# Kernel tuning notes

Measured on AMD Instinct MI355X. Metric: run time of the kernel, lower is better.

The kernel has to match this reference:

```python
import jax, jax.numpy as jnp
import numpy as np

B, Q, DIN, DOUT = 1, 1024, 4096, 4096
H, G, HD = 32, 8, 128          # heads, kv groups, head_dim; group_size = H // G
PREV = 3072                     # cached KV length
MAXPOS = 4096                   # rope table length (>= PREV + Q)
START = PREV


def _rope_tables(max_pos, head_dim):
    half = head_dim // 2
    inv_freq = 1.0 / (10000.0 ** (jnp.arange(half, dtype=jnp.float32) / half))
    ang = jnp.arange(max_pos, dtype=jnp.float32)[:, None] * inv_freq[None, :]
    ang = jnp.concatenate([ang, ang], axis=-1)  # [max_pos, head_dim]
    return jnp.cos(ang), jnp.sin(ang)


def apply_rope(x, cos, sin, start_pos):
    # x: [b, h, s, d]; rotate-half RoPE with absolute positions start_pos..start_pos+s
    s, d = x.shape[2], x.shape[3]
    c = cos[start_pos:start_pos + s]  # [s, d] (start_pos is a Python int)
    sn = sin[start_pos:start_pos + s]
    x1, x2 = x[..., : d // 2], x[..., d // 2:]
    rotated = jnp.concatenate([-x2, x1], axis=-1)
    return x * c + rotated * sn


def setup_inputs() -> dict:
    key = jax.random.key(0)
    ks = jax.random.split(key, 7)
    x = jax.random.normal(ks[0], (B, Q, DIN), dtype=jnp.float32)
    cos, sin = _rope_tables(MAXPOS, HD)
    # causal mask: query at abs position START+i may attend kv position j <= START+i
    qpos = START + jnp.arange(Q)
    kpos = jnp.arange(START + Q)
    mask = (kpos[None, :] > qpos[:, None])[None, None]  # [1,1,Q,KV], True = masked
    prev_k = jax.random.normal(ks[1], (B, G, PREV, HD), dtype=jnp.float32)
    prev_v = jax.random.normal(ks[2], (B, G, PREV, HD), dtype=jnp.float32)
    sc = 0.02
    Wq = jax.random.normal(ks[3], (DIN, DOUT), dtype=jnp.float32) * sc
    Wk = jax.random.normal(ks[4], (DIN, G * HD), dtype=jnp.float32) * sc
    Wv = jax.random.normal(ks[5], (DIN, G * HD), dtype=jnp.float32) * sc
    Wo = jax.random.normal(ks[6], (DOUT, DOUT), dtype=jnp.float32) * sc
    return dict(x=x, mask=mask, cos=cos, sin=sin, start_pos=START,
                prev_k=prev_k, prev_v=prev_v, Wq=Wq, Wk=Wk, Wv=Wv, Wo=Wo)


def reference(x, mask, cos, sin, start_pos, prev_k, prev_v, Wq, Wk, Wv, Wo):
    b, s, _ = x.shape
    gs = H // G  # group_size
    q = (x @ Wq).reshape(b, s, H, HD).transpose(0, 2, 1, 3)   # [b,H,s,hd]
    k = (x @ Wk).reshape(b, s, G, HD).transpose(0, 2, 1, 3)   # [b,G,s,hd]
    v = (x @ Wv).reshape(b, s, G, HD).transpose(0, 2, 1, 3)
    q = apply_rope(q, cos, sin, start_pos)
    k = apply_rope(k, cos, sin, start_pos)
    keys = jnp.concatenate([prev_k, k], axis=2)    # [b,G,KV,hd]
    values = jnp.concatenate([prev_v, v], axis=2)
    # grouped attention (equivalent to repeat_interleave of K/V over group_size)
    qg = q.reshape(b, G, gs, s, HD)
    scores = jnp.einsum('bgnqd,bgkd->bgnqk', qg, keys)        # [b,G,gs,s,KV]
    scores = jnp.where(mask[:, :, None], -jnp.inf, scores)
    attn = jax.nn.softmax(scores / np.sqrt(HD).astype(np.float32), axis=-1)
    ctx = jnp.einsum('bgnqk,bgkd->bgnqd', attn, values)       # [b,G,gs,s,hd]
    ctx = ctx.reshape(b, H, s, HD).transpose(0, 2, 1, 3).reshape(b, s, DOUT)
    out = ctx @ Wo
    return (out, keys, values)
```

## Files before the change

kernel.cpp:

```cpp
#include <hip/hip_runtime.h>
#include <hip/hip_bf16.h>

typedef unsigned short u16;
typedef unsigned int u32;
typedef __attribute__((ext_vector_type(4))) float f32x4;
typedef __attribute__((ext_vector_type(16))) float f32x16;
typedef __attribute__((ext_vector_type(8))) __bf16 bf16x8;
typedef __attribute__((ext_vector_type(4))) u16 u16x4;
typedef __attribute__((ext_vector_type(8))) u16 u16x8;
typedef __attribute__((ext_vector_type(4))) u32 u32x4;

#define START_POS 3072
#define NKV 4096
#define HD_ 128
#define SEQ 1024
#define DIN_ 4096
#define DQKV 6144

__device__ __forceinline__ void gll16(const void* g, void* l) {
  __builtin_amdgcn_global_load_lds((const __attribute__((address_space(1))) u32*)g,
                                   (__attribute__((address_space(3))) u32*)l, 16, 0, 0);
}
__device__ __forceinline__ u16 f2bf(float f) {
  u32 u = __builtin_bit_cast(u32, f);
  return (u16)((u + 0x7fffu + ((u >> 16) & 1u)) >> 16);
}
__device__ __forceinline__ u32 pack2bf(float a, float b) {
  __hip_bfloat162 t = __float22bfloat162_rn(float2{a, b});
  u32 u; __builtin_memcpy(&u, &t, 4);
  return u;
}
__device__ __forceinline__ f32x4 mfma16(bf16x8 a, bf16x8 b, f32x4 c) {
  return __builtin_amdgcn_mfma_f32_16x16x32_bf16(a, b, c, 0, 0, 0);
}
__device__ __forceinline__ f32x16 mfma32(bf16x8 a, bf16x8 b, f32x16 c) {
  return __builtin_amdgcn_mfma_f32_32x32x16_bf16(a, b, c, 0, 0, 0);
}

__global__ __launch_bounds__(256) void wtrans(const float* __restrict__ W,
    u16* __restrict__ Wt, int N, int ntn, int row_off)
{
  __shared__ float T[64][68];
  int bid = blockIdx.x;
  int nt = bid % ntn, kt = bid / ntn;
  int t = threadIdx.x;
  int kl = t >> 4, nl4 = (t & 15) << 2;
#pragma unroll
  for (int r = 0; r < 4; r++) {
    int row = r * 16 + kl;
    f32x4 v = *(const f32x4*)(W + (size_t)(kt * 64 + row) * N + nt * 64 + nl4);
    T[row][nl4] = v[0]; T[row][nl4 + 1] = v[1]; T[row][nl4 + 2] = v[2]; T[row][nl4 + 3] = v[3];
  }
  __syncthreads();
  int nl = t >> 2, k0 = (t & 3) << 4;
  u16x8 lo, hi;
#pragma unroll
  for (int j = 0; j < 8; j++) lo[j] = f2bf(T[k0 + j][nl]);
#pragma unroll
  for (int j = 0; j < 8; j++) hi[j] = f2bf(T[k0 + 8 + j][nl]);
  u16* dst = Wt + (size_t)(row_off + nt * 64 + nl) * 4096 + kt * 64 + k0;
  *(u16x8*)dst = lo;
  *(u16x8*)(dst + 8) = hi;
}

__global__ __launch_bounds__(256) void cvt_bf16(const float* __restrict__ src,
    u16* __restrict__ dst, int n4)
{
  int i = blockIdx.x * 256 + threadIdx.x;
  if (i >= n4) return;
  f32x4 v = *(const f32x4*)(src + (size_t)i * 4);
  u16x4 o;
#pragma unroll
  for (int j = 0; j < 4; j++) o[j] = f2bf(v[j]);
  *(u16x4*)(dst + (size_t)i * 4) = o;
}

__global__ __launch_bounds__(256) void gemm_bt(
    const u16* __restrict__ A, const u16* __restrict__ Bt,
    float* __restrict__ C, int N, int K, int nbx)
{
  __shared__ u16 As[2 * 128 * 64];
  __shared__ u16 Bs[2 * 64 * 64];
  int nwg = (int)gridDim.x;
  int orig = blockIdx.x;
  int q8 = nwg >> 3, r8 = nwg & 7;
  int xcd = orig & 7, jj = orig >> 3;
  int wgid = (xcd < r8 ? xcd * (q8 + 1) : r8 * (q8 + 1) + (xcd - r8) * q8) + jj;
  int by = wgid / nbx, bx = wgid % nbx;
  int tid = threadIdx.x, lane = tid & 63, wid = tid >> 6;
  int wr = wid >> 1, wc = wid & 1;
  int c = lane & 15, hh = lane >> 4;
  int srow = lane >> 3;
  int schunk = ((lane & 7) ^ srow) << 3;
  const u16* aS0 = A + (size_t)(by * 128 + wid * 32 + srow) * K + schunk;
  const u16* bS0 = Bt + (size_t)(bx * 64 + wid * 16 + srow) * K + schunk;

#define GSTAGE(buf, kk) do { \
  _Pragma("unroll") \
  for (int r = 0; r < 4; r++) \
    gll16(aS0 + (size_t)r * 8 * K + (kk), As + (buf) * 8192 + (wid * 32 + r * 8) * 64); \
  _Pragma("unroll") \
  for (int r = 0; r < 2; r++) \
    gll16(bS0 + (size_t)r * 8 * K + (kk), Bs + (buf) * 4096 + (wid * 16 + r * 8) * 64); \
} while (0)

  f32x4 acc[4][2] = {};
  int nk = K >> 6;
  int cur = 0;
  int rsl = c & 7;
  GSTAGE(0, 0);
  __syncthreads();
  for (int kt = 0; kt < nk; kt++) {
    if (kt + 1 < nk) GSTAGE(cur ^ 1, (kt + 1) * 64);
    const u16* Ab = As + cur * 8192;
    const u16* Bb = Bs + cur * 4096;
#pragma unroll
    for (int kk = 0; kk < 2; kk++) {
      int slot = ((kk * 4 + hh) ^ rsl) * 8;
      bf16x8 af[4], bf[2];
#pragma unroll
      for (int i = 0; i < 4; i++)
        af[i] = *(const bf16x8*)(Ab + (wr * 64 + i * 16 + c) * 64 + slot);
#pragma unroll
      for (int i = 0; i < 2; i++)
        bf[i] = *(const bf16x8*)(Bb + (wc * 32 + i * 16 + c) * 64 + slot);
      __builtin_amdgcn_s_setprio(1);
#pragma unroll
      for (int mi = 0; mi < 4; mi++)
#pragma unroll
        for (int ni = 0; ni < 2; ni++)
          acc[mi][ni] = mfma16(af[mi], bf[ni], acc[mi][ni]);
      __builtin_amdgcn_s_setprio(0);
    }
    __syncthreads();
    cur ^= 1;
  }
#undef GSTAGE
  int row0 = by * 128 + wr * 64 + hh * 4;
  int col0 = bx * 64 + wc * 32 + c;
#pragma unroll
  for (int mi = 0; mi < 4; mi++)
#pragma unroll
    for (int ni = 0; ni < 2; ni++)
#pragma unroll
      for (int i = 0; i < 4; i++)
        C[(size_t)(row0 + mi * 16 + i) * N + col0 + ni * 16] = acc[mi][ni][i];
}

__global__ __launch_bounds__(256) void rope_q(const float* __restrict__ qkv,
    const float* __restrict__ cosb, const float* __restrict__ sinb, u16* __restrict__ qb)
{
  const float C2 = 0.12751744f;
  int tid = blockIdx.x * 256 + threadIdx.x;
  int dq = tid & 15, h = (tid >> 4) & 31, s = tid >> 9;
  int d = dq << 2;
  const float* base = qkv + (size_t)s * DQKV + h * HD_ + d;
  f32x4 a = *(const f32x4*)base;
  f32x4 b2 = *(const f32x4*)(base + 64);
  f32x4 cc = *(const f32x4*)(cosb + (size_t)(START_POS + s) * HD_ + d);
  f32x4 sn = *(const f32x4*)(sinb + (size_t)(START_POS + s) * HD_ + d);
  u16x4 o1, o2;
#pragma unroll
  for (int i = 0; i < 4; i++) {
    o1[i] = f2bf((a[i] * cc[i] - b2[i] * sn[i]) * C2);
    o2[i] = f2bf((b2[i] * cc[i] + a[i] * sn[i]) * C2);
  }
  u16* dst = qb + ((size_t)h * SEQ + s) * HD_ + d;
  *(u16x4*)dst = o1;
  *(u16x4*)(dst + 64) = o2;
}

__global__ __launch_bounds__(256) void rope_k(const float* __restrict__ qkv,
    const float* __restrict__ cosb, const float* __restrict__ sinb,
    float* __restrict__ keys, u16* __restrict__ kbb)
{
  int tid = blockIdx.x * 256 + threadIdx.x;
  int dq = tid & 15, g = (tid >> 4) & 7, s = tid >> 7;
  int d = dq << 2;
  const float* base = qkv + (size_t)s * DQKV + DIN_ + g * HD_ + d;
  f32x4 a = *(const f32x4*)base;
  f32x4 b2 = *(const f32x4*)(base + 64);
  f32x4 cc = *(const f32x4*)(cosb + (size_t)(START_POS + s) * HD_ + d);
  f32x4 sn = *(const f32x4*)(sinb + (size_t)(START_POS + s) * HD_ + d);
  f32x4 o1, o2;
  u16x4 p1, p2;
#pragma unroll
  for (int i = 0; i < 4; i++) {
    o1[i] = a[i] * cc[i] - b2[i] * sn[i];
    o2[i] = b2[i] * cc[i] + a[i] * sn[i];
    p1[i] = f2bf(o1[i]);
    p2[i] = f2bf(o2[i]);
  }
  size_t off = ((size_t)g * NKV + START_POS + s) * HD_ + d;
  *(f32x4*)(keys + off) = o1;
  *(f32x4*)(keys + off + 64) = o2;
  *(u16x4*)(kbb + off) = p1;
  *(u16x4*)(kbb + off + 64) = p2;
}

__global__ __launch_bounds__(256) void copy_vnew(const float* __restrict__ qkv,
    float* __restrict__ values)
{
  int tid = blockIdx.x * 256 + threadIdx.x;
  int dq = tid & 31, g = (tid >> 5) & 7, s = tid >> 8;
  int d = dq << 2;
  f32x4 v = *(const f32x4*)(qkv + (size_t)s * DQKV + DIN_ + 1024 + g * HD_ + d);
  *(f32x4*)(values + ((size_t)g * NKV + START_POS + s) * HD_ + d) = v;
}

__global__ __launch_bounds__(256) void prev_copy(const float* __restrict__ pk,
    const float* __restrict__ pv, float* __restrict__ keys, float* __restrict__ values,
    u16* __restrict__ kbb)
{
  int idx = blockIdx.x * 256 + threadIdx.x;
  int d4 = idx & 31;
  int rest = idx >> 5;
  int p = rest % 3072, g = rest / 3072;
  f32x4 kq = *(const f32x4*)(pk + (size_t)idx * 4);
  f32x4 vq = *(const f32x4*)(pv + (size_t)idx * 4);
  size_t off = ((size_t)g * NKV + p) * HD_ + d4 * 4;
  *(f32x4*)(keys + off) = kq;
  *(f32x4*)(values + off) = vq;
  u16x4 kb4;
#pragma unroll
  for (int i = 0; i < 4; i++) kb4[i] = f2bf(kq[i]);
  *(u16x4*)(kbb + off) = kb4;
}

__global__ __launch_bounds__(256) void vtrans(const float* __restrict__ pv,
    const float* __restrict__ qkv, u16* __restrict__ vT)
{
  __shared__ float T[64][68];
  int bid = blockIdx.x;
  int dt = bid & 1, pt = (bid >> 1) & 63, g = bid >> 7;
  int t = threadIdx.x;
  int pl = t >> 4, dl4 = (t & 15) << 2;
#pragma unroll
  for (int r = 0; r < 4; r++) {
    int row = r * 16 + pl;
    int pos = pt * 64 + row;
    f32x4 v;
    if (pos < START_POS)
      v = *(const f32x4*)(pv + ((size_t)g * START_POS + pos) * HD_ + dt * 64 + dl4);
    else
      v = *(const f32x4*)(qkv + (size_t)(pos - START_POS) * DQKV + 5120 + g * HD_ + dt * 64 + dl4);
    T[row][dl4] = v[0]; T[row][dl4 + 1] = v[1]; T[row][dl4 + 2] = v[2]; T[row][dl4 + 3] = v[3];
  }
  __syncthreads();
  int dl = t >> 2, p0 = (t & 3) << 4;
  u16x8 lo, hi;
#pragma unroll
  for (int j = 0; j < 8; j++) lo[j] = f2bf(T[p0 + j][dl]);
#pragma unroll
  for (int j = 0; j < 8; j++) hi[j] = f2bf(T[p0 + 8 + j][dl]);
  u16* dst = vT + ((size_t)g * HD_ + dt * 64 + dl) * NKV + pt * 64 + p0;
  *(u16x8*)dst = lo;
  *(u16x8*)(dst + 8) = hi;
}

__global__ __launch_bounds__(128, 2) void attn_fwd(
    const u16* __restrict__ qb, const u16* __restrict__ kb,
    const u16* __restrict__ vT, float* __restrict__ Opart, float* __restrict__ Ml)
{
  __shared__ u16 Ks[2 * 32 * 128];
  __shared__ u16 Vs[2 * 128 * 32];
  int bid = blockIdx.x;
  int g = bid & 7, j = bid >> 3;
  int sp = j >> 6, jj = j & 63;
  int h = g * 4 + (jj >> 4), qt = jj & 15;
  int tid = threadIdx.x, lane = tid & 63, w = tid >> 6;
  int c32 = lane & 31, h8 = lane >> 5;
  int qw0 = qt * 64 + w * 32;
  bf16x8 Qf[8];
#pragma unroll
  for (int dc = 0; dc < 8; dc++)
    Qf[dc] = *(const bf16x8*)(qb + ((size_t)(h * 1024 + qw0 + c32)) * 128 + dc * 16 + h8 * 8);
  f32x16 O0 = {}, O1 = {}, O2 = {}, O3 = {};
  float Mx = -1e30f, Ls = 0.f;
  int t0 = sp ? (49 + qt) : 0;
  int t1 = sp ? (98 + 2 * qt) : (49 + qt);

#define STAGE_KV(tt, bo) do { \
  _Pragma("unroll") \
  for (int r = 0; r < 4; r++) { \
    int s = w * 256 + r * 64 + lane; \
    int krow = s >> 4, sl = s & 15; \
    gll16(kb + ((size_t)(g * 4096 + (tt) * 32 + krow)) * 128 + (sl ^ (krow & 7)) * 8, \
          Ks + (bo) + (w * 256 + r * 64) * 8); \
    int d = s >> 2, sl2 = s & 3; \
    gll16(vT + ((size_t)(g * 128 + d)) * 4096 + (tt) * 32 + (sl2 ^ ((d >> 1) & 3)) * 8, \
          Vs + (bo) + (w * 256 + r * 64) * 8); \
  } \
} while (0)

  int cur = 0;
  STAGE_KV(t0, 0);
  __syncthreads();
  int vxr = (c32 >> 1) & 3;
  for (int t = t0; t < t1; t++) {
    if (t + 1 < t1) STAGE_KV(t + 1, (cur ^ 1) * 4096);
    const u16* Kb = Ks + cur * 4096;
    const u16* Vb = Vs + cur * 4096;
    f32x16 S0 = {}, Sb = {};
    __builtin_amdgcn_s_setprio(1);
#pragma unroll
    for (int dc = 0; dc < 8; dc += 2) {
      int sxA = (2 * dc + h8) ^ (c32 & 7);
      int sxB = (2 * dc + 2 + h8) ^ (c32 & 7);
      bf16x8 kA = *(const bf16x8*)(Kb + (size_t)c32 * 128 + sxA * 8);
      bf16x8 kB = *(const bf16x8*)(Kb + (size_t)c32 * 128 + sxB * 8);
      S0 = mfma32(kA, Qf[dc], S0);
      Sb = mfma32(kB, Qf[dc + 1], Sb);
    }
    __builtin_amdgcn_s_setprio(0);
#pragma unroll
    for (int r = 0; r < 16; r++) S0[r] += Sb[r];
    if (t * 32 + 31 > START_POS + qw0) {
      int qa = START_POS + qw0 + c32;
#pragma unroll
      for (int r = 0; r < 16; r++) {
        int kvo = t * 32 + (r & 3) + 8 * (r >> 2) + 4 * h8;
        if (kvo > qa) S0[r] = -1e30f;
      }
    }
    float tm[16];
#pragma unroll
    for (int r = 0; r < 16; r++) tm[r] = S0[r];
#pragma unroll
    for (int sft = 8; sft >= 1; sft >>= 1)
#pragma unroll
      for (int r = 0; r < sft; r++) tm[r] = fmaxf(tm[r], tm[r + sft]);
    float full = fmaxf(tm[0], __shfl_xor(tm[0], 32));
    if (!__all(full <= Mx + 8.0f)) {
      float Mn = fmaxf(Mx, full);
      float al = exp2f(Mx - Mn);
      Mx = Mn;
      Ls *= al;
#pragma unroll
      for (int r = 0; r < 16; r++) { O0[r] *= al; O1[r] *= al; O2[r] *= al; O3[r] *= al; }
    }
#pragma unroll
    for (int r = 0; r < 16; r++) S0[r] = exp2f(S0[r] - Mx);
    float ts[16];
#pragma unroll
    for (int r = 0; r < 16; r++) ts[r] = S0[r];
#pragma unroll
    for (int sft = 8; sft >= 1; sft >>= 1)
#pragma unroll
      for (int r = 0; r < sft; r++) ts[r] = ts[r] + ts[r + sft];
    Ls += ts[0] + __shfl_xor(ts[0], 32);
    u32 pk0[8], x0[8];
#pragma unroll
    for (int m = 0; m < 8; m++) pk0[m] = pack2bf(S0[2 * m], S0[2 * m + 1]);
#pragma unroll
    for (int m = 0; m < 8; m++) x0[m] = __shfl_xor(pk0[m], 32);
    bf16x8 pbf[2];
    {
      u32x4 f0 = { h8 ? x0[2] : pk0[0], h8 ? x0[3] : pk0[1],
                   h8 ? pk0[2] : x0[0], h8 ? pk0[3] : x0[1] };
      u32x4 f1 = { h8 ? x0[6] : pk0[4], h8 ? x0[7] : pk0[5],
                   h8 ? pk0[6] : x0[4], h8 ? pk0[7] : x0[5] };
      pbf[0] = __builtin_bit_cast(bf16x8, f0);
      pbf[1] = __builtin_bit_cast(bf16x8, f1);
    }
    __builtin_amdgcn_s_setprio(1);
#pragma unroll
    for (int kc = 0; kc < 2; kc++) {
      int sv = 2 * kc + h8;
      int sx = (sv ^ vxr) * 8;
      {
        bf16x8 vf = *(const bf16x8*)(Vb + (size_t)(0 * 32 + c32) * 32 + sx);
        O0 = mfma32(vf, pbf[kc], O0);
      }
      {
        bf16x8 vf = *(const bf16x8*)(Vb + (size_t)(1 * 32 + c32) * 32 + sx);
        O1 = mfma32(vf, pbf[kc], O1);
      }
      {
        bf16x8 vf = *(const bf16x8*)(Vb + (size_t)(2 * 32 + c32) * 32 + sx);
        O2 = mfma32(vf, pbf[kc], O2);
      }
      {
        bf16x8 vf = *(const bf16x8*)(Vb + (size_t)(3 * 32 + c32) * 32 + sx);
        O3 = mfma32(vf, pbf[kc], O3);
      }
    }
    __builtin_amdgcn_s_setprio(0);
    __syncthreads();
    cur ^= 1;
  }
#undef STAGE_KV
  {
    float* Orow = Opart + (size_t)sp * 4194304 + (size_t)(qw0 + c32) * 4096 + h * 128;
#pragma unroll
    for (int a = 0; a < 4; a++) {
      f32x4 o0, o1, o2, o3;
#pragma unroll
      for (int b = 0; b < 4; b++) {
        o0[b] = O0[4 * a + b]; o1[b] = O1[4 * a + b];
        o2[b] = O2[4 * a + b]; o3[b] = O3[4 * a + b];
      }
      int d0 = 8 * a + 4 * h8;
      *(f32x4*)(Orow + d0) = o0;
      *(f32x4*)(Orow + 32 + d0) = o1;
      *(f32x4*)(Orow + 64 + d0) = o2;
      *(f32x4*)(Orow + 96 + d0) = o3;
    }
    if (h8 == 0) {
      float* mp = Ml + ((size_t)(sp * 32 + h) * 1024 + qw0 + c32) * 2;
      mp[0] = Mx; mp[1] = Ls;
    }
  }
}

__global__ __launch_bounds__(256) void attn_combine(const float* __restrict__ Opart,
    const float* __restrict__ Ml, u16* __restrict__ ctxb)
{
  int idx = blockIdx.x * 256 + threadIdx.x;
  int q = idx >> 10, c4 = idx & 1023;
  int col = c4 * 4, h = col >> 7;
  const float* m0p = Ml + ((size_t)h * 1024 + q) * 2;
  const float* m1p = Ml + ((size_t)(32 + h) * 1024 + q) * 2;
  float m0 = m0p[0], l0 = m0p[1];
  float m1 = m1p[0], l1 = m1p[1];
  float M = fmaxf(m0, m1);
  float w0 = exp2f(m0 - M);
  float w1 = exp2f(m1 - M);
  float inv = 1.0f / (l0 * w0 + l1 * w1);
  f32x4 a = *(const f32x4*)(Opart + (size_t)q * 4096 + col);
  f32x4 b = *(const f32x4*)(Opart + 4194304 + (size_t)q * 4096 + col);
  u16x4 o;
#pragma unroll
  for (int i = 0; i < 4; i++) o[i] = f2bf((a[i] * w0 + b[i] * w1) * inv);
  *(u16x4*)(ctxb + (size_t)q * 4096 + col) = o;
}

extern "C" void kernel_launch(void* const* d_in, const int* in_sizes, int n_in,
                              void* d_out, int out_size, void* d_ws, size_t ws_size,
                              hipStream_t stream) {
  const float* x      = (const float*)d_in[0];
  const float* cosb   = (const float*)d_in[2];
  const float* sinb   = (const float*)d_in[3];
  const float* prev_k = (const float*)d_in[5];
  const float* prev_v = (const float*)d_in[6];
  const float* Wq     = (const float*)d_in[7];
  const float* Wk     = (const float*)d_in[8];
  const float* Wv     = (const float*)d_in[9];
  const float* Wo     = (const float*)d_in[10];

  u16* Wt_proj = (u16*)d_ws;
  u16* Wt_out  = Wt_proj + (size_t)6144 * 4096;
  u16* xb      = Wt_out + (size_t)4096 * 4096;
  float* qkv   = (float*)(xb + (size_t)1024 * 4096);
  u16* qb      = (u16*)(qkv + (size_t)1024 * 6144);
  u16* kbb     = qb + (size_t)32 * 1024 * 128;
  u16* vT      = kbb + (size_t)8 * 4096 * 128;
  u16* ctxb    = vT + (size_t)8 * 4096 * 128;
  float* Opart = (float*)d_ws;
  float* Ml    = Opart + (size_t)2 * 1024 * 4096;

  float* outp   = (float*)d_out;
  float* keys   = outp + (size_t)4194304;
  float* values = outp + (size_t)8388608;

  wtrans<<<4096, 256, 0, stream>>>(Wq, Wt_proj, 4096, 64, 0);
  wtrans<<<1024, 256, 0, stream>>>(Wk, Wt_proj, 1024, 16, 4096);
  wtrans<<<1024, 256, 0, stream>>>(Wv, Wt_proj, 1024, 16, 5120);
  wtrans<<<4096, 256, 0, stream>>>(Wo, Wt_out, 4096, 64, 0);
  cvt_bf16<<<4096, 256, 0, stream>>>(x, xb, 1048576);

  gemm_bt<<<768, 256, 0, stream>>>(xb, Wt_proj, qkv, 6144, 4096, 96);

  rope_q<<<2048, 256, 0, stream>>>(qkv, cosb, sinb, qb);
  rope_k<<<512, 256, 0, stream>>>(qkv, cosb, sinb, keys, kbb);
  copy_vnew<<<1024, 256, 0, stream>>>(qkv, values);
  prev_copy<<<3072, 256, 0, stream>>>(prev_k, prev_v, keys, values, kbb);
  vtrans<<<1024, 256, 0, stream>>>(prev_v, qkv, vT);

  attn_fwd<<<1024, 128, 0, stream>>>(qb, kbb, vT, Opart, Ml);
  attn_combine<<<4096, 256, 0, stream>>>(Opart, Ml, ctxb);

  gemm_bt<<<512, 256, 0, stream>>>(ctxb, Wt_out, outp, 4096, 4096, 64);
}
```

Baseline: 345.8 us.

## Widen attention blocks to 4 waves and split KV into four balanced chunks

The attention kernel now runs 4 waves per block over a 128-query tile, so each staged K/V tile in shared memory is reused by twice as many query rows. The KV range for each tile is split into four roughly equal chunks instead of two, which keeps the grid at 1024 blocks. The combine kernel merges four partial results using log-sum-exp weights. Partial outputs and statistics are placed in the workspace, partly reusing the qkv buffer, which is dead by that point. This trades more partial-result traffic in the combine step for more K/V reuse and better load balance.

```diff
diff --git a/kernel.cpp b/kernel.cpp
--- a/kernel.cpp
+++ b/kernel.cpp
@@ -258,38 +258,40 @@
   *(u16x8*)(dst + 8) = hi;
 }
 
-__global__ __launch_bounds__(128, 2) void attn_fwd(
+__global__ __launch_bounds__(256, 2) void attn_fwd(
     const u16* __restrict__ qb, const u16* __restrict__ kb,
-    const u16* __restrict__ vT, float* __restrict__ Opart, float* __restrict__ Ml)
+    const u16* __restrict__ vT, float* __restrict__ OpA, float* __restrict__ OpB,
+    float* __restrict__ Ml)
 {
   __shared__ u16 Ks[2 * 32 * 128];
   __shared__ u16 Vs[2 * 128 * 32];
   int bid = blockIdx.x;
   int g = bid & 7, j = bid >> 3;
-  int sp = j >> 6, jj = j & 63;
-  int h = g * 4 + (jj >> 4), qt = jj & 15;
+  int sp = j >> 5, jj = j & 31;
+  int h = g * 4 + (jj >> 3), qt = jj & 7;
   int tid = threadIdx.x, lane = tid & 63, w = tid >> 6;
   int c32 = lane & 31, h8 = lane >> 5;
-  int qw0 = qt * 64 + w * 32;
+  int qw0 = qt * 128 + w * 32;
   bf16x8 Qf[8];
 #pragma unroll
   for (int dc = 0; dc < 8; dc++)
     Qf[dc] = *(const bf16x8*)(qb + ((size_t)(h * 1024 + qw0 + c32)) * 128 + dc * 16 + h8 * 8);
   f32x16 O0 = {}, O1 = {}, O2 = {}, O3 = {};
   float Mx = -1e30f, Ls = 0.f;
-  int t0 = sp ? (49 + qt) : 0;
-  int t1 = sp ? (98 + 2 * qt) : (49 + qt);
+  int T = 100 + 4 * qt;
+  int t0 = (sp * T) >> 2;
+  int t1 = ((sp + 1) * T) >> 2;
 
 #define STAGE_KV(tt, bo) do { \
   _Pragma("unroll") \
-  for (int r = 0; r < 4; r++) { \
-    int s = w * 256 + r * 64 + lane; \
+  for (int r = 0; r < 2; r++) { \
+    int s = r * 256 + w * 64 + lane; \
     int krow = s >> 4, sl = s & 15; \
     gll16(kb + ((size_t)(g * 4096 + (tt) * 32 + krow)) * 128 + (sl ^ (krow & 7)) * 8, \
-          Ks + (bo) + (w * 256 + r * 64) * 8); \
+          Ks + (bo) + (r * 256 + w * 64) * 8); \
     int d = s >> 2, sl2 = s & 3; \
     gll16(vT + ((size_t)(g * 128 + d)) * 4096 + (tt) * 32 + (sl2 ^ ((d >> 1) & 3)) * 8, \
-          Vs + (bo) + (w * 256 + r * 64) * 8); \
+          Vs + (bo) + (r * 256 + w * 64) * 8); \
   } \
 } while (0)
 
@@ -391,7 +393,8 @@
   }
 #undef STAGE_KV
   {
-    float* Orow = Opart + (size_t)sp * 4194304 + (size_t)(qw0 + c32) * 4096 + h * 128;
+    float* Obase = (sp < 3) ? (OpA + (size_t)sp * 4194304) : OpB;
+    float* Orow = Obase + (size_t)(qw0 + c32) * 4096 + h * 128;
 #pragma unroll
     for (int a = 0; a < 4; a++) {
       f32x4 o0, o1, o2, o3;
@@ -413,25 +416,32 @@
   }
 }
 
-__global__ __launch_bounds__(256) void attn_combine(const float* __restrict__ Opart,
-    const float* __restrict__ Ml, u16* __restrict__ ctxb)
+__global__ __launch_bounds__(256) void attn_combine(const float* __restrict__ OpA,
+    const float* __restrict__ OpB, const float* __restrict__ Ml, u16* __restrict__ ctxb)
 {
   int idx = blockIdx.x * 256 + threadIdx.x;
   int q = idx >> 10, c4 = idx & 1023;
   int col = c4 * 4, h = col >> 7;
-  const float* m0p = Ml + ((size_t)h * 1024 + q) * 2;
-  const float* m1p = Ml + ((size_t)(32 + h) * 1024 + q) * 2;
-  float m0 = m0p[0], l0 = m0p[1];
-  float m1 = m1p[0], l1 = m1p[1];
-  float M = fmaxf(m0, m1);
-  float w0 = exp2f(m0 - M);
-  float w1 = exp2f(m1 - M);
-  float inv = 1.0f / (l0 * w0 + l1 * w1);
-  f32x4 a = *(const f32x4*)(Opart + (size_t)q * 4096 + col);
-  f32x4 b = *(const f32x4*)(Opart + 4194304 + (size_t)q * 4096 + col);
+  float m[4], l[4];
+#pragma unroll
+  for (int s = 0; s < 4; s++) {
+    const float* mp = Ml + ((size_t)(s * 32 + h) * 1024 + q) * 2;
+    m[s] = mp[0]; l[s] = mp[1];
+  }
+  float M = fmaxf(fmaxf(m[0], m[1]), fmaxf(m[2], m[3]));
+  float wgt[4];
+  float den = 0.f;
+#pragma unroll
+  for (int s = 0; s < 4; s++) { wgt[s] = exp2f(m[s] - M); den += l[s] * wgt[s]; }
+  float inv = 1.0f / den;
+  f32x4 a0 = *(const f32x4*)(OpA + (size_t)q * 4096 + col);
+  f32x4 a1 = *(const f32x4*)(OpA + 4194304 + (size_t)q * 4096 + col);
+  f32x4 a2 = *(const f32x4*)(OpA + 2 * 4194304 + (size_t)q * 4096 + col);
+  f32x4 a3 = *(const f32x4*)(OpB + (size_t)q * 4096 + col);
   u16x4 o;
 #pragma unroll
-  for (int i = 0; i < 4; i++) o[i] = f2bf((a[i] * w0 + b[i] * w1) * inv);
+  for (int i = 0; i < 4; i++)
+    o[i] = f2bf((a0[i] * wgt[0] + a1[i] * wgt[1] + a2[i] * wgt[2] + a3[i] * wgt[3]) * inv);
   *(u16x4*)(ctxb + (size_t)q * 4096 + col) = o;
 }
 
@@ -456,8 +466,9 @@
   u16* kbb     = qb + (size_t)32 * 1024 * 128;
   u16* vT      = kbb + (size_t)8 * 4096 * 128;
   u16* ctxb    = vT + (size_t)8 * 4096 * 128;
-  float* Opart = (float*)d_ws;
-  float* Ml    = Opart + (size_t)2 * 1024 * 4096;
+  float* OpA = (float*)d_ws;
+  float* OpB = qkv;
+  float* Ml  = qkv + (size_t)4194304;
 
   float* outp   = (float*)d_out;
   float* keys   = outp + (size_t)4194304;
@@ -477,8 +488,8 @@
   prev_copy<<<3072, 256, 0, stream>>>(prev_k, prev_v, keys, values, kbb);
   vtrans<<<1024, 256, 0, stream>>>(prev_v, qkv, vT);
 
-  attn_fwd<<<1024, 128, 0, stream>>>(qb, kbb, vT, Opart, Ml);
-  attn_combine<<<4096, 256, 0, stream>>>(Opart, Ml, ctxb);
+  attn_fwd<<<1024, 256, 0, stream>>>(qb, kbb, vT, OpA, OpB, Ml);
+  attn_combine<<<4096, 256, 0, stream>>>(OpA, OpB, Ml, ctxb);
 
   gemm_bt<<<512, 256, 0, stream>>>(ctxb, Wt_out, outp, 4096, 4096, 64);
 }
```

Measured after the change: 345.7 us. No clear change (-0.0%).
